# Kernel optimization log

Measured on AMD Instinct MI355X. Metric: run time of the kernel, lower is better.

## Reference

```python
import jax, jax.numpy as jnp
import numpy as np

H, HD, RD = 16, 128, 64          # n_heads, head_dim, rope_dim
CD = HD - RD                      # content_dim = 64
THETA = 10000.0


def apply_rope(x, cos, sin):
    # x: [B,H,T,RD]; cos/sin: [T,RD//2] broadcast over B,H
    d = x.shape[-1] // 2
    x1, x2 = x[..., :d], x[..., d:]
    return jnp.concatenate([x1 * cos - x2 * sin, x1 * sin + x2 * cos], axis=-1)


def setup_inputs() -> dict:
    key = jax.random.key(0)
    ks = jax.random.split(key, 9)
    d_model, q_rank, d_latent = 2048, 512, 512
    B, T = 2, 2048
    s = 0.02
    return {
        "x": jax.random.normal(ks[0], (B, T, d_model), dtype=jnp.float32),
        "Wq_down": jax.random.normal(ks[1], (d_model, q_rank), dtype=jnp.float32) * s,
        "Wq_up": jax.random.normal(ks[2], (q_rank, H * CD), dtype=jnp.float32) * s,
        "Wq_rope": jax.random.normal(ks[3], (d_model, H * RD), dtype=jnp.float32) * s,
        "Wkv_down": jax.random.normal(ks[4], (d_model, d_latent), dtype=jnp.float32) * s,
        "Wk_up": jax.random.normal(ks[5], (d_latent, H * CD), dtype=jnp.float32) * s,
        "Wv_up": jax.random.normal(ks[6], (d_latent, H * HD), dtype=jnp.float32) * s,
        "Wk_rope": jax.random.normal(ks[7], (d_model, H * RD), dtype=jnp.float32) * s,
        "Wo": jax.random.normal(ks[8], (H * HD, d_model), dtype=jnp.float32) * s,
    }


def reference(x, Wq_down, Wq_up, Wq_rope, Wkv_down, Wk_up, Wv_up, Wk_rope, Wo):
    B, T, _ = x.shape

    # low-rank projections
    q_content = (x @ Wq_down) @ Wq_up            # [B,T,H*CD]
    q_pos = x @ Wq_rope                          # [B,T,H*RD]
    kv_latent = x @ Wkv_down                     # [B,T,d_latent]
    k_content = kv_latent @ Wk_up                # [B,T,H*CD]
    k_pos = x @ Wk_rope                          # [B,T,H*RD]
    v = kv_latent @ Wv_up                        # [B,T,H*HD]

    def split_heads(t, d):
        return t.reshape(B, T, H, d).transpose(0, 2, 1, 3)  # [B,H,T,d]

    q_content = split_heads(q_content, CD)
    q_pos = split_heads(q_pos, RD)
    k_content = split_heads(k_content, CD)
    k_pos = split_heads(k_pos, RD)
    v = split_heads(v, HD)

    # rotary tables: [T, RD//2]
    inv_freq = 1.0 / (THETA ** (jnp.arange(0, RD, 2, dtype=jnp.float32) / RD))
    freqs = jnp.arange(T, dtype=jnp.float32)[:, None] * inv_freq[None, :]
    cos, sin = jnp.cos(freqs), jnp.sin(freqs)

    q_pos = apply_rope(q_pos, cos, sin)
    k_pos = apply_rope(k_pos, cos, sin)

    q = jnp.concatenate([q_content, q_pos], axis=-1)  # [B,H,T,HD]
    k = jnp.concatenate([k_content, k_pos], axis=-1)  # [B,H,T,HD]

    # causal SDPA, scale = 1/sqrt(head_dim)
    scale = 1.0 / jnp.sqrt(jnp.asarray(HD, dtype=q.dtype))
    scores = jnp.einsum("bhqd,bhkd->bhqk", q, k) * scale
    causal = jnp.tril(jnp.ones((T, T), dtype=bool))
    scores = jnp.where(causal, scores, jnp.finfo(scores.dtype).min)
    attn = jax.nn.softmax(scores, axis=-1)
    out = jnp.einsum("bhqk,bhkd->bhqd", attn, v)      # [B,H,T,HD]

    out = out.transpose(0, 2, 1, 3).reshape(B, T, H * HD)
    return out @ Wo
```

## Files before the change

kernel.cpp:

```cpp
#include <hip/hip_runtime.h>
#include <hip/hip_bf16.h>
#include <stdint.h>
#include <math.h>

#define H_ 16
#define HD_ 128
#define RD_ 64
#define CD_ 64
#define DM_ 2048
#define QR_ 512
#define DL_ 512
#define B_ 2
#define T_ 2048
#define M_TOT (B_*T_)

typedef __attribute__((ext_vector_type(8))) short short8;
typedef __attribute__((ext_vector_type(4))) float f32x4;
typedef __attribute__((ext_vector_type(16))) float f32x16;

__device__ __forceinline__ unsigned short f2b_hw(float f){
  __hip_bfloat16 h = __float2bfloat16(f);
  union { __hip_bfloat16 h; unsigned short u; } c; c.h = h; return c.u;
}
__device__ __forceinline__ float b2f(unsigned short b){
  union { unsigned u; float f; } a; a.u = ((unsigned)b) << 16;
  return a.f;
}
__device__ __forceinline__ unsigned pack2(float lo, float hi){
  __hip_bfloat162 h2 = __float22bfloat162_rn(make_float2(lo, hi));
  union { __hip_bfloat162 h; unsigned u; } c; c.h = h2; return c.u;
}

#define GLOAD16(g, l) __builtin_amdgcn_global_load_lds( \
    (__attribute__((address_space(1))) void*)(g), \
    (__attribute__((address_space(3))) void*)(l), 16, 0, 0)

__global__ void cast_f32_bf16(const float* __restrict__ src,
                              unsigned short* __restrict__ dst, int n){
  int i = (blockIdx.x * blockDim.x + threadIdx.x) * 4;
  if (i < n){
    float4 v = *(const float4*)(src + i);
    ushort4 o;
    o.x = f2b_hw(v.x); o.y = f2b_hw(v.y); o.z = f2b_hw(v.z); o.w = f2b_hw(v.w);
    *(ushort4*)(dst + i) = o;
  }
}

__global__ void rope_table(float2* __restrict__ tab){
  int idx = blockIdx.x * 256 + threadIdx.x;
  int t = idx >> 5, j = idx & 31;
  float invf = exp2f(-(float)j * 0.4152410118750f);
  float fr = (float)t * invf;
  float s, c;
  sincosf(fr, &s, &c);
  tab[idx] = make_float2(c, s);
}

struct TTe { const float* src; unsigned short* dst; int K, N, blk0; };
struct TT8 { TTe e[8]; };

__global__ void transpose_cast8(TT8 tab){
  __shared__ float tile[32][33];
  int bid = blockIdx.x;
  const float* src = tab.e[0].src;
  unsigned short* dst = tab.e[0].dst;
  int K = tab.e[0].K, N = tab.e[0].N, loc = bid;
  #pragma unroll
  for (int j = 1; j < 8; j++){
    if (bid >= tab.e[j].blk0){
      src = tab.e[j].src; dst = tab.e[j].dst;
      K = tab.e[j].K; N = tab.e[j].N; loc = bid - tab.e[j].blk0;
    }
  }
  int cols = N / 32;
  int n0 = (loc % cols) * 32, k0 = (loc / cols) * 32;
  int tx = threadIdx.x, ty = threadIdx.y;
  #pragma unroll
  for (int r = ty; r < 32; r += 8)
    tile[r][tx] = src[(size_t)(k0 + r) * N + n0 + tx];
  __syncthreads();
  #pragma unroll
  for (int r = ty; r < 32; r += 8)
    dst[(size_t)(n0 + r) * K + k0 + tx] = f2b_hw(tile[tx][r]);
}

template<int MODE>
__global__ __launch_bounds__(256) void gemm_bt(
    const unsigned short* __restrict__ A, int lda,
    const unsigned short* __restrict__ Bt,
    void* __restrict__ Cv, int ldc, int N, int K)
{
  __shared__ unsigned short As[128 * 32];
  __shared__ unsigned short Bs[128 * 32];
  int tid = threadIdx.x;

  int gx = gridDim.x;
  int nwg = gx * gridDim.y;
  int lin = blockIdx.x + gx * blockIdx.y;
  int q8 = nwg >> 3;
  int nl = (lin & 7) * q8 + (lin >> 3);
  int m0 = (nl / gx) * 128, n0 = (nl % gx) * 128;

  int lane = tid & 63, w = tid >> 6;
  int wr = (w >> 1) * 64, wc = (w & 1) * 64;
  int mr = lane & 15, kg = lane >> 4;

  const unsigned short* Ag = A  + (size_t)(m0 + (tid >> 2)) * lda + ((tid & 3) << 3);
  const unsigned short* Bg = Bt + (size_t)(n0 + (tid >> 2)) * K + ((tid & 3) << 3);

  f32x4 acc[4][4];
  #pragma unroll
  for (int i = 0; i < 4; i++)
    #pragma unroll
    for (int j = 0; j < 4; j++)
      acc[i][j] = (f32x4){0.f, 0.f, 0.f, 0.f};

  for (int k0 = 0; k0 < K; k0 += 32) {
    #pragma unroll
    for (int j = 0; j < 2; j++) {
      GLOAD16(Ag + (size_t)j * 64 * lda, &As[j * 2048 + tid * 8]);
      GLOAD16(Bg + (size_t)j * 64 * K, &Bs[j * 2048 + tid * 8]);
    }
    Ag += 32; Bg += 32;
    __syncthreads();
    short8 af[4], bf[4];
    #pragma unroll
    for (int i = 0; i < 4; i++)
      af[i] = *(const short8*)&As[(wr + i * 16 + mr) * 32 + kg * 8];
    #pragma unroll
    for (int j = 0; j < 4; j++)
      bf[j] = *(const short8*)&Bs[(wc + j * 16 + mr) * 32 + kg * 8];
    __builtin_amdgcn_s_setprio(1);
    #pragma unroll
    for (int i = 0; i < 4; i++)
      #pragma unroll
      for (int j = 0; j < 4; j++)
        acc[i][j] = __builtin_amdgcn_mfma_f32_16x16x32_bf16(af[i], bf[j], acc[i][j], 0, 0, 0);
    __builtin_amdgcn_s_setprio(0);
    __syncthreads();
  }

  if (MODE == 1) {
    float* C = (float*)Cv;
    #pragma unroll
    for (int i = 0; i < 4; i++)
      #pragma unroll
      for (int j = 0; j < 4; j++)
        #pragma unroll
        for (int r = 0; r < 4; r++) {
          int row = m0 + wr + i * 16 + kg * 4 + r;
          int col = n0 + wc + j * 16 + mr;
          C[(size_t)row * ldc + col] = acc[i][j][r];
        }
  }
}

template<int MODE>
__global__ __launch_bounds__(512, 1) void gemm256(
    const unsigned short* __restrict__ A, int lda,
    const unsigned short* __restrict__ Bt,
    void* __restrict__ Cv, void* __restrict__ Cv2, void* __restrict__ Cv3,
    const float2* __restrict__ tab,
    int ldc, int N, int K)
{
  __shared__ __align__(16) unsigned short lds[65536];
  char* ldsb = (char*)lds;

  const int tid = threadIdx.x;
  const int lane = tid & 63, w = tid >> 6;
  const int wm = w >> 2, wn = w & 3;
  const int l15 = lane & 15, kg = lane >> 4;

  int gx = gridDim.x;
  int nwg = gx * gridDim.y;
  int lin = blockIdx.x + gx * blockIdx.y;
  int q8 = nwg >> 3;
  int nl = (lin & 7) * q8 + (lin >> 3);
  int m0 = (nl / gx) * 256, n0 = (nl % gx) * 256;

  const unsigned short* Aeff = A;
  if (MODE == 5 && n0 >= 1024) Aeff = A + 512;

  const int srow = tid >> 3;
  const int scol = ((((tid & 7) << 4) ^ (((tid >> 5) & 1) << 5)) >> 1);
  const int aswz = ((l15 >> 2) & 1) << 5;

#define STG(bufb, kt) do {                                                     \
    int k0_ = (kt) * 64;                                                       \
    _Pragma("unroll")                                                          \
    for (int h_ = 0; h_ < 2; h_++)                                             \
      _Pragma("unroll")                                                        \
      for (int i_ = 0; i_ < 2; i_++) {                                         \
        GLOAD16(Aeff + (size_t)(m0 + h_*128 + i_*64 + srow) * lda + k0_ + scol,\
                ldsb + (bufb)*65536 + h_*16384 + i_*8192 + tid*16);            \
        GLOAD16(Bt + (size_t)(n0 + h_*128 + i_*64 + srow) * K + k0_ + scol,    \
                ldsb + (bufb)*65536 + 32768 + h_*16384 + i_*8192 + tid*16);    \
      }                                                                        \
  } while (0)

  f32x4 acc[8][4];
  #pragma unroll
  for (int i = 0; i < 8; i++)
    #pragma unroll
    for (int j = 0; j < 4; j++)
      acc[i][j] = (f32x4){0.f, 0.f, 0.f, 0.f};

  const int nK = K >> 6;
  STG(0, 0);
  STG(1, 1);

  for (int t = 0; t < nK; t++) {
    const int c = t & 1;
    if (t < nK - 1) { asm volatile("s_waitcnt vmcnt(8)" ::: "memory"); }
    else            { asm volatile("s_waitcnt vmcnt(0)" ::: "memory"); }
    __builtin_amdgcn_s_barrier();
    __builtin_amdgcn_sched_barrier(0);

    const char* bufA = ldsb + c * 65536 + wm * 16384;
    const char* bufB = ldsb + c * 65536 + 32768;

    short8 bfr[4][2];
    #pragma unroll
    for (int nf = 0; nf < 4; nf++) {
      int nr = wn * 64 + nf * 16 + l15;
      #pragma unroll
      for (int kk = 0; kk < 2; kk++) {
        int L = (nr & 127) * 128 + kk * 64 + kg * 16;
        bfr[nf][kk] = *(const short8*)(bufB + (nr >> 7) * 16384 + (L ^ aswz));
      }
    }
    __builtin_amdgcn_s_setprio(1);
    #pragma unroll
    for (int mh = 0; mh < 2; mh++) {
      short8 afr[4][2];
      #pragma unroll
      for (int q = 0; q < 4; q++) {
        int mf = mh * 4 + q;
        #pragma unroll
        for (int kk = 0; kk < 2; kk++) {
          int L = (mf * 16 + l15) * 128 + kk * 64 + kg * 16;
          afr[q][kk] = *(const short8*)(bufA + (L ^ aswz));
        }
      }
      #pragma unroll
      for (int q = 0; q < 4; q++)
        #pragma unroll
        for (int nf = 0; nf < 4; nf++)
          #pragma unroll
          for (int kk = 0; kk < 2; kk++)
            acc[mh*4+q][nf] = __builtin_amdgcn_mfma_f32_16x16x32_bf16(
                afr[q][kk], bfr[nf][kk], acc[mh*4+q][nf], 0, 0, 0);
    }
    __builtin_amdgcn_s_setprio(0);
    __builtin_amdgcn_sched_barrier(0);
    __builtin_amdgcn_s_barrier();
    __builtin_amdgcn_sched_barrier(0);
    if (t + 2 < nK) STG(c, t + 2);
  }
#undef STG

  if (MODE == 4) {
    if (n0 < 1024) {
      unsigned short* C = (unsigned short*)Cv;
      #pragma unroll
      for (int mf = 0; mf < 8; mf++)
        #pragma unroll
        for (int nf = 0; nf < 4; nf++)
          #pragma unroll
          for (int rr = 0; rr < 4; rr++) {
            int row = m0 + wm * 128 + mf * 16 + kg * 4 + rr;
            int col = n0 + wn * 64 + nf * 16 + l15;
            C[(size_t)row * ldc + col] = f2b_hw(acc[mf][nf][rr]);
          }
    } else {
      const bool isq = (n0 < 2048);
      unsigned short* dst = (unsigned short*)(isq ? Cv2 : Cv3);
      int hbase = ((n0 - (isq ? 1024 : 2048)) >> 6) + wn;
      #pragma unroll
      for (int nf = 0; nf < 2; nf++) {
        int jr = nf * 16 + l15;
        #pragma unroll
        for (int mf = 0; mf < 8; mf++)
          #pragma unroll
          for (int rr = 0; rr < 4; rr++) {
            int gr = m0 + wm * 128 + mf * 16 + kg * 4 + rr;
            int tt = gr & (T_ - 1), bb = gr >> 11;
            float2 cs = tab[tt * 32 + jr];
            float x1 = acc[mf][nf][rr], x2 = acc[mf][nf + 2][rr];
            size_t base = ((size_t)(bb * H_ + hbase) * T_ + tt) * 128 + 64;
            dst[base + jr]      = f2b_hw(x1 * cs.x - x2 * cs.y);
            dst[base + jr + 32] = f2b_hw(x1 * cs.y + x2 * cs.x);
          }
      }
    }
  } else {
    if (n0 < 2048) {
      unsigned short* dstp = (unsigned short*)(n0 < 1024 ? Cv : Cv2);
      int cb0 = n0 - (n0 < 1024 ? 0 : 1024);
      #pragma unroll
      for (int nf = 0; nf < 4; nf++) {
        int colb = cb0 + wn * 64 + nf * 16 + l15;
        int h = colb >> 6, d = colb & 63;
        #pragma unroll
        for (int mf = 0; mf < 8; mf++)
          #pragma unroll
          for (int rr = 0; rr < 4; rr++) {
            int gr = m0 + wm * 128 + mf * 16 + kg * 4 + rr;
            size_t idx = ((size_t)((gr >> 11) * H_ + h) * T_ + (gr & (T_-1))) * 128 + d;
            dstp[idx] = f2b_hw(acc[mf][nf][rr]);
          }
      }
    } else {
      unsigned short* vtp = (unsigned short*)Cv3;
      #pragma unroll
      for (int nf = 0; nf < 4; nf++) {
        int c2 = n0 + wn * 64 + nf * 16 + l15 - 2048;
        int h = c2 >> 7, d = c2 & 127;
        #pragma unroll
        for (int mf = 0; mf < 8; mf++) {
          int gr0 = m0 + wm * 128 + mf * 16 + kg * 4;
          int bb = gr0 >> 11, t0 = gr0 & (T_-1);
          ushort4 o;
          o.x = f2b_hw(acc[mf][nf][0]); o.y = f2b_hw(acc[mf][nf][1]);
          o.z = f2b_hw(acc[mf][nf][2]); o.w = f2b_hw(acc[mf][nf][3]);
          *(ushort4*)&vtp[((size_t)(bb * H_ + h) * 128 + d) * T_ + t0] = o;
        }
      }
    }
  }
}

__global__ __launch_bounds__(256, 2) void attn_fwd7(
    const unsigned short* __restrict__ qh,
    const unsigned short* __restrict__ kh,
    const unsigned short* __restrict__ vt,
    unsigned short* __restrict__ ao)
{
  __shared__ __align__(16) unsigned short lds[4 * 8192];

  const int tid  = threadIdx.x;
  const int lane = tid & 63, w = tid >> 6;
  const int l31  = lane & 31, hi = lane >> 5;
  const int bh = blockIdx.y;
  const int b  = bh >> 4, hd = bh & 15;
  int qt = blockIdx.x;
  if (bh >= 16) qt = 15 - qt;
  const int q0w   = qt * 128 + w * 32;
  const int qg    = q0w + l31;
  const int qmaxw = q0w + 31;
  const int nt    = 2 * qt + 2;

  const unsigned short* Qg = qh + (size_t)bh * T_ * 128;
  const unsigned short* Kg = kh + (size_t)bh * T_ * 128;
  const unsigned short* Vg = vt + (size_t)bh * 128 * T_;

  short8 qf[8];
  #pragma unroll
  for (int kc = 0; kc < 8; kc++)
    qf[kc] = *(const short8*)&Qg[(size_t)qg * 128 + kc * 16 + hi * 8];

  f32x16 accO[4];
  #pragma unroll
  for (int sb = 0; sb < 4; sb++)
    #pragma unroll
    for (int r = 0; r < 16; r++) accO[sb][r] = 0.f;

  float m = -1e30f, lsum = 0.f;
  const float SC = 0.12751743f;

  int krow[4], kwof[4], vrow[4], vwof[4];
  #pragma unroll
  for (int jj = 0; jj < 4; jj++){
    int r_ = (w * 4 + jj) * 4 + (lane >> 4);
    krow[jj] = r_;
    kwof[jj] = r_ * 128 + ((((lane & 15) * 16) ^ ((r_ & 7) << 4)) >> 1);
    int d_ = (w * 4 + jj) * 8 + (lane >> 3);
    vrow[jj] = d_;
    vwof[jj] = d_ * 64 + ((((lane & 7) * 16) ^ ((d_ & 7) << 4)) >> 1);
  }
  const int kcol = (lane & 15) * 8;
  const int vcol = (lane & 7) * 8;

  uint4 kst[4], vst[4];

#define REG_LOAD(kvt) do {                                                    \
    int kv0s = (kvt) * 64;                                                    \
    _Pragma("unroll")                                                         \
    for (int j_ = 0; j_ < 4; j_++) {                                          \
      kst[j_] = *(const uint4*)&Kg[(size_t)(kv0s + krow[j_]) * 128 + kcol];   \
      vst[j_] = *(const uint4*)&Vg[(size_t)vrow[j_] * T_ + kv0s + vcol];      \
    }                                                                         \
  } while (0)

#define DS_WRITE(bufi) do {                                                   \
    unsigned short* ksb_ = lds + (bufi) * 8192;                               \
    unsigned short* vsb_ = lds + 16384 + (bufi) * 8192;                       \
    _Pragma("unroll")                                                         \
    for (int j_ = 0; j_ < 4; j_++) {                                          \
      *(uint4*)&ksb_[kwof[j_]] = kst[j_];                                     \
      *(uint4*)&vsb_[vwof[j_]] = vst[j_];                                     \
    }                                                                         \
  } while (0)

  REG_LOAD(0);
  DS_WRITE(0);
  if (nt > 1) REG_LOAD(1);
  asm volatile("s_waitcnt lgkmcnt(0)" ::: "memory");
  __builtin_amdgcn_s_barrier();
  __builtin_amdgcn_sched_barrier(0);

  for (int t = 0; t < nt; t++) {
    const int cur = t & 1;
    if (t + 1 < nt) DS_WRITE(cur ^ 1);
    if (t + 2 < nt) REG_LOAD(t + 2);
    const int kv0 = t * 64;
    if (kv0 <= qmaxw) {
      const unsigned short* Kb = lds + cur * 8192;
      const unsigned short* Vb = lds + 16384 + cur * 8192;

      f32x16 sa0, sa1;
      #pragma unroll
      for (int r = 0; r < 16; r++) { sa0[r] = 0.f; sa1[r] = 0.f; }
      __builtin_amdgcn_s_setprio(1);
      #pragma unroll
      for (int kc = 0; kc < 8; kc++) {
        int co = (kc * 32 + hi * 16);
        int r0 = l31;
        short8 kf0 = *(const short8*)&Kb[r0 * 128 + ((co ^ ((r0 & 7) << 4)) >> 1)];
        sa0 = __builtin_amdgcn_mfma_f32_32x32x16_bf16(kf0, qf[kc], sa0, 0, 0, 0);
        int r1 = 32 + l31;
        short8 kf1 = *(const short8*)&Kb[r1 * 128 + ((co ^ ((r1 & 7) << 4)) >> 1)];
        sa1 = __builtin_amdgcn_mfma_f32_32x32x16_bf16(kf1, qf[kc], sa1, 0, 0, 0);
      }
      __builtin_amdgcn_s_setprio(0);

      float p0[16], p1[16];
      float pmax = -1e30f;
      bool needMask = (kv0 + 63 > q0w);
      if (needMask) {
        #pragma unroll
        for (int r = 0; r < 16; r++) {
          int crow = (r & 3) + 8 * (r >> 2) + 4 * hi;
          float v0 = sa0[r] * SC;
          float v1 = sa1[r] * SC;
          if (kv0 + crow > qg)      v0 = -1e30f;
          if (kv0 + 32 + crow > qg) v1 = -1e30f;
          p0[r] = v0; p1[r] = v1;
          pmax = fmaxf(pmax, fmaxf(v0, v1));
        }
      } else {
        #pragma unroll
        for (int r = 0; r < 16; r++) {
          float v0 = sa0[r] * SC;
          float v1 = sa1[r] * SC;
          p0[r] = v0; p1[r] = v1;
          pmax = fmaxf(pmax, fmaxf(v0, v1));
        }
      }
      pmax = fmaxf(pmax, __shfl_xor(pmax, 32, 64));
      if (!__all(pmax <= m + 8.f)) {
        float mn  = fmaxf(m, pmax);
        float fac = exp2f(m - mn);
        m = mn;
        lsum *= fac;
        #pragma unroll
        for (int sb = 0; sb < 4; sb++)
          #pragma unroll
          for (int r = 0; r < 16; r++) accO[sb][r] *= fac;
      }
      float ls = 0.f;
      #pragma unroll
      for (int r = 0; r < 16; r++) {
        p0[r] = exp2f(p0[r] - m);
        p1[r] = exp2f(p1[r] - m);
        ls += p0[r] + p1[r];
      }
      ls += __shfl_xor(ls, 32, 64);
      lsum += ls;

      #pragma unroll
      for (int kc2 = 0; kc2 < 4; kc2++) {
        unsigned A01, A23, B01, B23;
        if (kc2 == 0) { A01 = pack2(p0[0], p0[1]);  A23 = pack2(p0[2], p0[3]);
                        B01 = pack2(p0[4], p0[5]);  B23 = pack2(p0[6], p0[7]); }
        else if (kc2 == 1) { A01 = pack2(p0[8], p0[9]);   A23 = pack2(p0[10], p0[11]);
                             B01 = pack2(p0[12], p0[13]); B23 = pack2(p0[14], p0[15]); }
        else if (kc2 == 2) { A01 = pack2(p1[0], p1[1]);  A23 = pack2(p1[2], p1[3]);
                             B01 = pack2(p1[4], p1[5]);  B23 = pack2(p1[6], p1[7]); }
        else { A01 = pack2(p1[8], p1[9]);   A23 = pack2(p1[10], p1[11]);
               B01 = pack2(p1[12], p1[13]); B23 = pack2(p1[14], p1[15]); }
        asm("v_permlane32_swap_b32 %0, %1" : "+v"(A01), "+v"(B01));
        asm("v_permlane32_swap_b32 %0, %1" : "+v"(A23), "+v"(B23));
        union { unsigned u[4]; short8 v; } pk;
        pk.u[0] = A01; pk.u[1] = A23; pk.u[2] = B01; pk.u[3] = B23;
        short8 pa = pk.v;
        __builtin_amdgcn_s_setprio(1);
        #pragma unroll
        for (int sb = 0; sb < 4; sb++) {
          int d = sb * 32 + l31;
          short8 vf = *(const short8*)&Vb[d * 64 + (((kc2 * 32 + hi * 16) ^ ((d & 7) << 4)) >> 1)];
          accO[sb] = __builtin_amdgcn_mfma_f32_32x32x16_bf16(vf, pa, accO[sb], 0, 0, 0);
        }
        __builtin_amdgcn_s_setprio(0);
      }
    }
    __builtin_amdgcn_sched_barrier(0);
    asm volatile("s_waitcnt lgkmcnt(0)" ::: "memory");
    __builtin_amdgcn_s_barrier();
    __builtin_amdgcn_sched_barrier(0);
  }

  float rl = 1.0f / lsum;
  size_t orow = ((size_t)b * T_ + qg) * (H_*HD_) + hd * 128;
  #pragma unroll
  for (int sb = 0; sb < 4; sb++)
    #pragma unroll
    for (int g = 0; g < 4; g++) {
      ushort4 o;
      o.x = f2b_hw(accO[sb][4 * g + 0] * rl);
      o.y = f2b_hw(accO[sb][4 * g + 1] * rl);
      o.z = f2b_hw(accO[sb][4 * g + 2] * rl);
      o.w = f2b_hw(accO[sb][4 * g + 3] * rl);
      *(ushort4*)&ao[orow + sb * 32 + 8 * g + 4 * hi] = o;
    }
#undef REG_LOAD
#undef DS_WRITE
}

extern "C" void kernel_launch(void* const* d_in, const int* in_sizes, int n_in,
                              void* d_out, int out_size, void* d_ws, size_t ws_size,
                              hipStream_t stream)
{
  (void)in_sizes; (void)n_in; (void)out_size; (void)ws_size;
  const float* x        = (const float*)d_in[0];
  const float* Wq_down  = (const float*)d_in[1];
  const float* Wq_up    = (const float*)d_in[2];
  const float* Wq_rope  = (const float*)d_in[3];
  const float* Wkv_down = (const float*)d_in[4];
  const float* Wk_up    = (const float*)d_in[5];
  const float* Wv_up    = (const float*)d_in[6];
  const float* Wk_rope  = (const float*)d_in[7];
  const float* Wo       = (const float*)d_in[8];

  char* ws = (char*)d_ws;
  unsigned short* xb      = (unsigned short*)(ws + 0);
  unsigned short* Wdall   = (unsigned short*)(ws + 16777216);
  unsigned short* WquT    = (unsigned short*)(ws + 29360128);
  unsigned short* WkcvT   = (unsigned short*)(ws + 30408704);
  unsigned short* WoT     = (unsigned short*)(ws + 33554432);
  unsigned short* projall = (unsigned short*)(ws + 41943040);
  unsigned short* qh      = (unsigned short*)(ws + 67108864);
  unsigned short* kh      = (unsigned short*)(ws + 83886080);
  unsigned short* vt      = (unsigned short*)(ws + 100663296);
  unsigned short* ao      = (unsigned short*)(ws + 117440512);
  float2*         ctab    = (float2*)(ws + 134217728);

  dim3 tb(32, 8);

  cast_f32_bf16<<<(M_TOT * DM_ / 4 + 255) / 256, 256, 0, stream>>>(x, xb, M_TOT * DM_);
  rope_table<<<256, 256, 0, stream>>>(ctab);

  TT8 tab;
  int blk = 0;
  tab.e[0] = { Wq_down,  Wdall,               DM_, QR_,     blk }; blk += (QR_/32)*(DM_/32);
  tab.e[1] = { Wkv_down, Wdall + 512*2048,    DM_, DL_,     blk }; blk += (DL_/32)*(DM_/32);
  tab.e[2] = { Wq_rope,  Wdall + 1024*2048,   DM_, H_*RD_,  blk }; blk += (H_*RD_/32)*(DM_/32);
  tab.e[3] = { Wk_rope,  Wdall + 2048*2048,   DM_, H_*RD_,  blk }; blk += (H_*RD_/32)*(DM_/32);
  tab.e[4] = { Wq_up,    WquT,                QR_, H_*CD_,  blk }; blk += (H_*CD_/32)*(QR_/32);
  tab.e[5] = { Wk_up,    WkcvT,               DL_, H_*CD_,  blk }; blk += (H_*CD_/32)*(DL_/32);
  tab.e[6] = { Wv_up,    WkcvT + 1024*512,    DL_, H_*HD_,  blk }; blk += (H_*HD_/32)*(DL_/32);
  tab.e[7] = { Wo,       WoT,                 H_*HD_, DM_,  blk }; blk += (DM_/32)*(H_*HD_/32);
  transpose_cast8<<<blk, tb, 0, stream>>>(tab);

  gemm256<4><<<dim3(3072/256, M_TOT/256), 512, 0, stream>>>(
      xb, DM_, Wdall, projall, qh, kh, ctab, 1024, 3072, DM_);
  gemm256<5><<<dim3(4096/256, M_TOT/256), 512, 0, stream>>>(
      projall, 1024, WquT, qh, kh, vt, nullptr, 0, 4096, DL_);

  attn_fwd7<<<dim3(16, 32), 256, 0, stream>>>(qh, kh, vt, ao);

  gemm_bt<1><<<dim3(DM_/128, M_TOT/128), 256, 0, stream>>>(
      ao, 2048, WoT, d_out, DM_, DM_, H_*HD_);
}
```

Baseline: 312.0 us.

## Replace output projection GEMM with double-buffered 128x256 swizzled-LDS kernel

The final Wo projection moves from a simple 128x128-tile kernel with one LDS buffer and a synchronous K loop to a new 512-thread kernel. The new kernel uses 128x256 tiles, K steps of 64, two LDS buffers that prefetch two stages ahead with explicit vmcnt waits, and XOR-swizzled LDS addressing to avoid bank conflicts. The aim is to hide global load latency and raise MFMA utilisation in this GEMM. In exchange it uses much more LDS (96 KB), allowing only one workgroup per CU, and launches 256 workgroups instead of 512.

New measurement: 301.4 us. 3.4% less time.

```diff
diff --git a/kernel.cpp b/kernel.cpp
--- a/kernel.cpp
+++ b/kernel.cpp
@@ -82,77 +82,6 @@
   #pragma unroll
   for (int r = ty; r < 32; r += 8)
     dst[(size_t)(n0 + r) * K + k0 + tx] = f2b_hw(tile[tx][r]);
-}
-
-template<int MODE>
-__global__ __launch_bounds__(256) void gemm_bt(
-    const unsigned short* __restrict__ A, int lda,
-    const unsigned short* __restrict__ Bt,
-    void* __restrict__ Cv, int ldc, int N, int K)
-{
-  __shared__ unsigned short As[128 * 32];
-  __shared__ unsigned short Bs[128 * 32];
-  int tid = threadIdx.x;
-
-  int gx = gridDim.x;
-  int nwg = gx * gridDim.y;
-  int lin = blockIdx.x + gx * blockIdx.y;
-  int q8 = nwg >> 3;
-  int nl = (lin & 7) * q8 + (lin >> 3);
-  int m0 = (nl / gx) * 128, n0 = (nl % gx) * 128;
-
-  int lane = tid & 63, w = tid >> 6;
-  int wr = (w >> 1) * 64, wc = (w & 1) * 64;
-  int mr = lane & 15, kg = lane >> 4;
-
-  const unsigned short* Ag = A  + (size_t)(m0 + (tid >> 2)) * lda + ((tid & 3) << 3);
-  const unsigned short* Bg = Bt + (size_t)(n0 + (tid >> 2)) * K + ((tid & 3) << 3);
-
-  f32x4 acc[4][4];
-  #pragma unroll
-  for (int i = 0; i < 4; i++)
-    #pragma unroll
-    for (int j = 0; j < 4; j++)
-      acc[i][j] = (f32x4){0.f, 0.f, 0.f, 0.f};
-
-  for (int k0 = 0; k0 < K; k0 += 32) {
-    #pragma unroll
-    for (int j = 0; j < 2; j++) {
-      GLOAD16(Ag + (size_t)j * 64 * lda, &As[j * 2048 + tid * 8]);
-      GLOAD16(Bg + (size_t)j * 64 * K, &Bs[j * 2048 + tid * 8]);
-    }
-    Ag += 32; Bg += 32;
-    __syncthreads();
-    short8 af[4], bf[4];
-    #pragma unroll
-    for (int i = 0; i < 4; i++)
-      af[i] = *(const short8*)&As[(wr + i * 16 + mr) * 32 + kg * 8];
-    #pragma unroll
-    for (int j = 0; j < 4; j++)
-      bf[j] = *(const short8*)&Bs[(wc + j * 16 + mr) * 32 + kg * 8];
-    __builtin_amdgcn_s_setprio(1);
-    #pragma unroll
-    for (int i = 0; i < 4; i++)
-      #pragma unroll
-      for (int j = 0; j < 4; j++)
-        acc[i][j] = __builtin_amdgcn_mfma_f32_16x16x32_bf16(af[i], bf[j], acc[i][j], 0, 0, 0);
-    __builtin_amdgcn_s_setprio(0);
-    __syncthreads();
-  }
-
-  if (MODE == 1) {
-    float* C = (float*)Cv;
-    #pragma unroll
-    for (int i = 0; i < 4; i++)
-      #pragma unroll
-      for (int j = 0; j < 4; j++)
-        #pragma unroll
-        for (int r = 0; r < 4; r++) {
-          int row = m0 + wr + i * 16 + kg * 4 + r;
-          int col = n0 + wc + j * 16 + mr;
-          C[(size_t)row * ldc + col] = acc[i][j][r];
-        }
-  }
 }
 
 template<int MODE>
@@ -328,6 +257,110 @@
       }
     }
   }
+}
+
+__global__ __launch_bounds__(512, 1) void gemm_out(
+    const unsigned short* __restrict__ A, int lda,
+    const unsigned short* __restrict__ Bt,
+    float* __restrict__ C, int ldc, int K)
+{
+  __shared__ __align__(16) unsigned short lds[49152];
+  char* ldsb = (char*)lds;
+
+  const int tid = threadIdx.x;
+  const int lane = tid & 63, w = tid >> 6;
+  const int wm = w >> 2, wn = w & 3;
+  const int l15 = lane & 15, kg = lane >> 4;
+
+  int gx = gridDim.x;
+  int nwg = gx * gridDim.y;
+  int lin = blockIdx.x + gx * blockIdx.y;
+  int q8 = nwg >> 3;
+  int nl = (lin & 7) * q8 + (lin >> 3);
+  int m0 = (nl / gx) * 128, n0 = (nl % gx) * 256;
+
+  const int srow = tid >> 3;
+  const int scol = ((((tid & 7) << 4) ^ (((tid >> 5) & 1) << 5)) >> 1);
+  const int aswz = ((l15 >> 2) & 1) << 5;
+
+#define STG(bufb, kt) do {                                                     \
+    int k0_ = (kt) * 64;                                                       \
+    _Pragma("unroll")                                                          \
+    for (int i_ = 0; i_ < 2; i_++)                                             \
+      GLOAD16(A + (size_t)(m0 + i_*64 + srow) * lda + k0_ + scol,              \
+              ldsb + (bufb)*49152 + i_*8192 + tid*16);                         \
+    _Pragma("unroll")                                                          \
+    for (int i_ = 0; i_ < 4; i_++)                                             \
+      GLOAD16(Bt + (size_t)(n0 + i_*64 + srow) * K + k0_ + scol,               \
+              ldsb + (bufb)*49152 + 16384 + i_*8192 + tid*16);                 \
+  } while (0)
+
+  f32x4 acc[4][4];
+  #pragma unroll
+  for (int i = 0; i < 4; i++)
+    #pragma unroll
+    for (int j = 0; j < 4; j++)
+      acc[i][j] = (f32x4){0.f, 0.f, 0.f, 0.f};
+
+  const int nK = K >> 6;
+  STG(0, 0);
+  STG(1, 1);
+
+  for (int t = 0; t < nK; t++) {
+    const int c = t & 1;
+    if (t < nK - 1) { asm volatile("s_waitcnt vmcnt(6)" ::: "memory"); }
+    else            { asm volatile("s_waitcnt vmcnt(0)" ::: "memory"); }
+    __builtin_amdgcn_s_barrier();
+    __builtin_amdgcn_sched_barrier(0);
+
+    const char* bufA = ldsb + c * 49152 + wm * 8192;
+    const char* bufB = ldsb + c * 49152 + 16384;
+
+    short8 bfr[4][2];
+    #pragma unroll
+    for (int nf = 0; nf < 4; nf++) {
+      int nr = wn * 64 + nf * 16 + l15;
+      #pragma unroll
+      for (int kk = 0; kk < 2; kk++) {
+        int L = (nr & 63) * 128 + kk * 64 + kg * 16;
+        bfr[nf][kk] = *(const short8*)(bufB + (nr >> 6) * 8192 + (L ^ aswz));
+      }
+    }
+    short8 afr[4][2];
+    #pragma unroll
+    for (int mf = 0; mf < 4; mf++)
+      #pragma unroll
+      for (int kk = 0; kk < 2; kk++) {
+        int L = (mf * 16 + l15) * 128 + kk * 64 + kg * 16;
+        afr[mf][kk] = *(const short8*)(bufA + (L ^ aswz));
+      }
+    __builtin_amdgcn_s_setprio(1);
+    #pragma unroll
+    for (int mf = 0; mf < 4; mf++)
+      #pragma unroll
+      for (int nf = 0; nf < 4; nf++)
+        #pragma unroll
+        for (int kk = 0; kk < 2; kk++)
+          acc[mf][nf] = __builtin_amdgcn_mfma_f32_16x16x32_bf16(
+              afr[mf][kk], bfr[nf][kk], acc[mf][nf], 0, 0, 0);
+    __builtin_amdgcn_s_setprio(0);
+    __builtin_amdgcn_sched_barrier(0);
+    __builtin_amdgcn_s_barrier();
+    __builtin_amdgcn_sched_barrier(0);
+    if (t + 2 < nK) STG(c, t + 2);
+  }
+#undef STG
+
+  #pragma unroll
+  for (int mf = 0; mf < 4; mf++)
+    #pragma unroll
+    for (int nf = 0; nf < 4; nf++)
+      #pragma unroll
+      for (int rr = 0; rr < 4; rr++) {
+        int row = m0 + wm * 64 + mf * 16 + kg * 4 + rr;
+        int col = n0 + wn * 64 + nf * 16 + l15;
+        C[(size_t)row * ldc + col] = acc[mf][nf][rr];
+      }
 }
 
 __global__ __launch_bounds__(256, 2) void attn_fwd7(
@@ -579,6 +612,6 @@
 
   attn_fwd7<<<dim3(16, 32), 256, 0, stream>>>(qh, kh, vt, ao);
 
-  gemm_bt<1><<<dim3(DM_/128, M_TOT/128), 256, 0, stream>>>(
-      ao, 2048, WoT, d_out, DM_, DM_, H_*HD_);
-}
+  gemm_out<<<dim3(DM_/256, M_TOT/128), 512, 0, stream>>>(
+      ao, 2048, WoT, (float*)d_out, DM_, H_*HD_);
+}
```
